# Kernel tuning notes

Measured on AMD Instinct MI355X. Metric: run time of the kernel, lower is better.

The kernel has to match this reference:

```python
import jax, jax.numpy as jnp
import numpy as np

N = 10000      # nodes (attention_adj_matrix_shape = (N, N))
E = 320000     # edges, avg degree 32
D_IN = 256     # input feature dim
D_H = 256      # hidden_units = [256]
ALPHA = 0.2    # leaky_relu slope for attention activation


def setup_inputs() -> dict:
    key = jax.random.key(0)
    k_x, k_src, k_dst, k_w1, k_b1, k_wa, k_ba = jax.random.split(key, 7)
    node_features = jax.random.normal(k_x, (N, D_IN), dtype=jnp.float32)
    # edges sorted by source column (tf.math.segment_sum requires sorted segment ids)
    src = jnp.sort(jax.random.randint(k_src, (E,), 0, N))
    dst = jax.random.randint(k_dst, (E,), 0, N)
    edges = jnp.stack([src, dst], axis=1).astype(jnp.int64)
    # hidden_layer: single Dense(256) (linear, keras Dense default activation=None)
    W1 = jax.random.normal(k_w1, (D_IN, D_H), dtype=jnp.float32) / np.sqrt(D_IN)
    b1 = jnp.zeros((D_H,), dtype=jnp.float32)
    # attention_layer: Dense(1) then activation
    Wa = jax.random.normal(k_wa, (2 * D_H, 1), dtype=jnp.float32) / np.sqrt(2 * D_H)
    ba = jnp.zeros((1,), dtype=jnp.float32)
    return {"node_features": node_features, "edges": edges,
            "W1": W1, "b1": b1, "Wa": Wa, "ba": ba}


def reference(node_features, edges, W1, b1, Wa, ba):
    n = node_features.shape[0]
    # hidden projection
    feats = node_features @ W1 + b1                       # [N, D_H]
    src, dst = edges[:, 0], edges[:, 1]
    # pairwise gather + concat: [E, 2*D_H]
    pair = jnp.concatenate([feats[src], feats[dst]], axis=1)
    scores = jax.nn.leaky_relu((pair @ Wa + ba)[:, 0], ALPHA)  # [E]
    # segment softmax over source node (matches exp / segment_sum / gather)
    ex = jnp.exp(scores)
    denom = jax.ops.segment_sum(ex, src, num_segments=n)       # [N]
    alpha = ex / denom[src]                                     # [E]
    # dense scatter of attention weights (scatter_nd sums duplicates)
    A = jnp.zeros((n, n), dtype=feats.dtype).at[src, dst].add(alpha)
    # add_self_features=False -> plain aggregate
    return A @ feats                                            # [N, D_H]
```

## Files before the change

### kernel.cpp

```cpp
#include <hip/hip_runtime.h>
#include <hip/hip_bf16.h>

#define N_NODES 10000
#define E_EDGES 320000
#define D 256
#define LRELU_ALPHA 0.2f


using short8  = __attribute__((ext_vector_type(8))) short;
using floatx4 = __attribute__((ext_vector_type(4))) float;
using bf16 = __hip_bfloat16;

__device__ __forceinline__ float bu2f(unsigned short u) {
    return __uint_as_float((unsigned)u << 16);
}

__global__ __launch_bounds__(256) void prep(const int* __restrict__ raw,
                                            int* __restrict__ dst,
                                            int* __restrict__ row_start) {
    bool is64 = true;
    #pragma unroll
    for (int t = 0; t < 16; ++t)
        if (raw[2 * t + 1] != 0) is64 = false;

    int e = blockIdx.x * 256 + threadIdx.x;
    if (e >= E_EDGES) return;
    int s, d, sprev;
    if (is64) { s = raw[4 * e]; d = raw[4 * e + 2]; sprev = e ? raw[4 * e - 4] : -1; }
    else      { s = raw[2 * e]; d = raw[2 * e + 1]; sprev = e ? raw[2 * e - 2] : -1; }
    dst[e] = d;
    for (int r = sprev + 1; r <= s; ++r) row_start[r] = e;
    if (e == E_EDGES - 1)
        for (int r = s + 1; r <= N_NODES; ++r) row_start[r] = E_EDGES;
}

__global__ __launch_bounds__(256) void xcast(const float* __restrict__ X,
                                             bf16* __restrict__ Xb) {
    const int i4 = blockIdx.x * 256 + threadIdx.x;
    const float4 v = ((const float4*)X)[i4];
    bf16* o = Xb + (size_t)i4 * 4;
    o[0] = __float2bfloat16(v.x);
    o[1] = __float2bfloat16(v.y);
    o[2] = __float2bfloat16(v.z);
    o[3] = __float2bfloat16(v.w);
}

__global__ __launch_bounds__(256) void wprep(const float* __restrict__ W1,
                                             bf16* __restrict__ W1f) {
    const int id = blockIdx.x * 256 + threadIdx.x;
    const int j = id & 7, l = (id >> 3) & 63, t = (id >> 9) & 15, s = id >> 13;
    const int k = s * 32 + (l >> 4) * 8 + j;
    const int n = t * 16 + (l & 15);
    W1f[id] = __float2bfloat16(W1[k * D + n]);
}

__global__ __launch_bounds__(256) void gemm_mfma(const bf16* __restrict__ Xb,
                                                 const bf16* __restrict__ W1f,
                                                 const float* __restrict__ b1,
                                                 const float* __restrict__ Wa,
                                                 bf16* __restrict__ featsb,
                                                 float* __restrict__ a_src,
                                                 float* __restrict__ a_dst) {
    const int w = threadIdx.x >> 6, l = threadIdx.x & 63;
    const int quad = l >> 4, lan = l & 15;
    const int row0 = blockIdx.x * 16;

    floatx4 acc[4] = {{0.f, 0.f, 0.f, 0.f}, {0.f, 0.f, 0.f, 0.f},
                      {0.f, 0.f, 0.f, 0.f}, {0.f, 0.f, 0.f, 0.f}};

    const short8* A8 = (const short8*)(Xb + (size_t)(row0 + lan) * D);
    const short8* B8 = (const short8*)W1f;

    #pragma unroll
    for (int s = 0; s < 8; ++s) {
        const short8 af = A8[s * 4 + quad];
        #pragma unroll
        for (int t = 0; t < 4; ++t) {
            const short8 bf = B8[(s * 16 + (4 * w + t)) * 64 + l];
            acc[t] = __builtin_amdgcn_mfma_f32_16x16x32_bf16(af, bf, acc[t], 0, 0, 0);
        }
    }

    float p1[4] = {0.f, 0.f, 0.f, 0.f}, p2[4] = {0.f, 0.f, 0.f, 0.f};
    #pragma unroll
    for (int t = 0; t < 4; ++t) {
        const int n = (4 * w + t) * 16 + lan;
        const float bias = b1[n], wa1 = Wa[n], wa2 = Wa[D + n];
        #pragma unroll
        for (int r = 0; r < 4; ++r) {
            const float v = acc[t][r] + bias;
            featsb[(size_t)(row0 + quad * 4 + r) * D + n] = __float2bfloat16(v);
            p1[r] += v * wa1;
            p2[r] += v * wa2;
        }
    }

    __shared__ float red1[4][16], red2[4][16];
    #pragma unroll
    for (int r = 0; r < 4; ++r) {
        #pragma unroll
        for (int off = 1; off < 16; off <<= 1) {
            p1[r] += __shfl_xor(p1[r], off);
            p2[r] += __shfl_xor(p2[r], off);
        }
        if (lan == 0) { red1[w][quad * 4 + r] = p1[r]; red2[w][quad * 4 + r] = p2[r]; }
    }
    __syncthreads();
    if (threadIdx.x < 16) {
        const int m = threadIdx.x;
        a_src[row0 + m] = red1[0][m] + red1[1][m] + red1[2][m] + red1[3][m];
        a_dst[row0 + m] = red2[0][m] + red2[1][m] + red2[2][m] + red2[3][m];
    }
}

__global__ __launch_bounds__(256) void aggregate(const int* __restrict__ dst,
                                                 const int* __restrict__ row_start,
                                                 const float* __restrict__ a_src,
                                                 const float* __restrict__ a_dst,
                                                 const float* __restrict__ ba,
                                                 const unsigned short* __restrict__ featsb,
                                                 float* __restrict__ out) {
    const int i = blockIdx.x * 4 + (threadIdx.x >> 6);
    const int l = threadIdx.x & 63;
    const int rs = row_start[i], re = row_start[i + 1];
    const float base = a_src[i] + ba[0];
    const ushort4* F = (const ushort4*)featsb;

    float4 acc = {0.f, 0.f, 0.f, 0.f};
    float dsum = 0.f;

    int e = rs;
    for (; e + 4 <= re; e += 4) {
        const int d0 = dst[e], d1 = dst[e + 1], d2 = dst[e + 2], d3 = dst[e + 3];
        const ushort4 f0 = F[(size_t)d0 * 64 + l];
        const ushort4 f1 = F[(size_t)d1 * 64 + l];
        const ushort4 f2 = F[(size_t)d2 * 64 + l];
        const ushort4 f3 = F[(size_t)d3 * 64 + l];
        float s0 = base + a_dst[d0]; s0 = (s0 > 0.f) ? s0 : LRELU_ALPHA * s0;
        float s1 = base + a_dst[d1]; s1 = (s1 > 0.f) ? s1 : LRELU_ALPHA * s1;
        float s2 = base + a_dst[d2]; s2 = (s2 > 0.f) ? s2 : LRELU_ALPHA * s2;
        float s3 = base + a_dst[d3]; s3 = (s3 > 0.f) ? s3 : LRELU_ALPHA * s3;
        const float x0 = expf(s0), x1 = expf(s1), x2 = expf(s2), x3 = expf(s3);
        acc.x += x0 * bu2f(f0.x) + x1 * bu2f(f1.x) + x2 * bu2f(f2.x) + x3 * bu2f(f3.x);
        acc.y += x0 * bu2f(f0.y) + x1 * bu2f(f1.y) + x2 * bu2f(f2.y) + x3 * bu2f(f3.y);
        acc.z += x0 * bu2f(f0.z) + x1 * bu2f(f1.z) + x2 * bu2f(f2.z) + x3 * bu2f(f3.z);
        acc.w += x0 * bu2f(f0.w) + x1 * bu2f(f1.w) + x2 * bu2f(f2.w) + x3 * bu2f(f3.w);
        dsum += x0 + x1 + x2 + x3;
    }
    for (; e < re; ++e) {
        const int d = dst[e];
        const ushort4 f = F[(size_t)d * 64 + l];
        float s = base + a_dst[d]; s = (s > 0.f) ? s : LRELU_ALPHA * s;
        const float x = expf(s);
        acc.x += x * bu2f(f.x); acc.y += x * bu2f(f.y);
        acc.z += x * bu2f(f.z); acc.w += x * bu2f(f.w);
        dsum += x;
    }

    const float inv = (re > rs) ? 1.f / dsum : 0.f;
    float4 o;
    o.x = acc.x * inv; o.y = acc.y * inv; o.z = acc.z * inv; o.w = acc.w * inv;
    ((float4*)out)[(size_t)i * 64 + l] = o;
}

extern "C" void kernel_launch(void* const* d_in, const int* in_sizes, int n_in,
                              void* d_out, int out_size, void* d_ws, size_t ws_size,
                              hipStream_t stream) {
    const float* X     = (const float*)d_in[0];
    const int*   edges = (const int*)d_in[1];
    const float* W1    = (const float*)d_in[2];
    const float* b1    = (const float*)d_in[3];
    const float* Wa    = (const float*)d_in[4];
    const float* ba    = (const float*)d_in[5];
    float* out = (float*)d_out;

    bf16* featsb = (bf16*)d_ws;
    bf16* Xb     = featsb + (size_t)N_NODES * D;
    bf16* W1f    = Xb + (size_t)N_NODES * D;
    float* a_src = (float*)(W1f + 65536);
    float* a_dst = a_src + N_NODES;
    int*   dstv  = (int*)(a_dst + N_NODES);
    int*   row_start = dstv + E_EDGES;

    prep<<<(E_EDGES + 255) / 256, 256, 0, stream>>>(edges, dstv, row_start);
    xcast<<<(N_NODES * D / 4) / 256, 256, 0, stream>>>(X, Xb);
    wprep<<<65536 / 256, 256, 0, stream>>>(W1, W1f);
    gemm_mfma<<<N_NODES / 16, 256, 0, stream>>>(Xb, W1f, b1, Wa, featsb, a_src, a_dst);
    aggregate<<<N_NODES / 4, 256, 0, stream>>>(dstv, row_start, a_src, a_dst, ba,
                                               (const unsigned short*)featsb, out);
}
```

Measured before the change: 112.1 us.

## Fuse X bf16 cast into GEMM and split aggregation into two feature halves

```diff
diff --git a/kernel.cpp b/kernel.cpp
--- a/kernel.cpp
+++ b/kernel.cpp
@@ -13,6 +13,11 @@
 
 __device__ __forceinline__ float bu2f(unsigned short u) {
     return __uint_as_float((unsigned)u << 16);
+}
+__device__ __forceinline__ unsigned short f2bu(float f) {
+    union { bf16 b; unsigned short u; } cv;
+    cv.b = __float2bfloat16(f);
+    return cv.u;
 }
 
 __global__ __launch_bounds__(256) void prep(const int* __restrict__ raw,
@@ -34,17 +39,6 @@
         for (int r = s + 1; r <= N_NODES; ++r) row_start[r] = E_EDGES;
 }
 
-__global__ __launch_bounds__(256) void xcast(const float* __restrict__ X,
-                                             bf16* __restrict__ Xb) {
-    const int i4 = blockIdx.x * 256 + threadIdx.x;
-    const float4 v = ((const float4*)X)[i4];
-    bf16* o = Xb + (size_t)i4 * 4;
-    o[0] = __float2bfloat16(v.x);
-    o[1] = __float2bfloat16(v.y);
-    o[2] = __float2bfloat16(v.z);
-    o[3] = __float2bfloat16(v.w);
-}
-
 __global__ __launch_bounds__(256) void wprep(const float* __restrict__ W1,
                                              bf16* __restrict__ W1f) {
     const int id = blockIdx.x * 256 + threadIdx.x;
@@ -54,7 +48,7 @@
     W1f[id] = __float2bfloat16(W1[k * D + n]);
 }
 
-__global__ __launch_bounds__(256) void gemm_mfma(const bf16* __restrict__ Xb,
+__global__ __launch_bounds__(256) void gemm_mfma(const float* __restrict__ X,
                                                  const bf16* __restrict__ W1f,
                                                  const float* __restrict__ b1,
                                                  const float* __restrict__ Wa,
@@ -68,12 +62,18 @@
     floatx4 acc[4] = {{0.f, 0.f, 0.f, 0.f}, {0.f, 0.f, 0.f, 0.f},
                       {0.f, 0.f, 0.f, 0.f}, {0.f, 0.f, 0.f, 0.f}};
 
-    const short8* A8 = (const short8*)(Xb + (size_t)(row0 + lan) * D);
+    const float4* Ax = (const float4*)(X + (size_t)(row0 + lan) * D);
     const short8* B8 = (const short8*)W1f;
 
     #pragma unroll
     for (int s = 0; s < 8; ++s) {
-        const short8 af = A8[s * 4 + quad];
+        const float4 u = Ax[s * 8 + quad * 2];
+        const float4 v = Ax[s * 8 + quad * 2 + 1];
+        short8 af;
+        af[0] = (short)f2bu(u.x); af[1] = (short)f2bu(u.y);
+        af[2] = (short)f2bu(u.z); af[3] = (short)f2bu(u.w);
+        af[4] = (short)f2bu(v.x); af[5] = (short)f2bu(v.y);
+        af[6] = (short)f2bu(v.z); af[7] = (short)f2bu(v.w);
         #pragma unroll
         for (int t = 0; t < 4; ++t) {
             const short8 bf = B8[(s * 16 + (4 * w + t)) * 64 + l];
@@ -113,54 +113,59 @@
     }
 }
 
-__global__ __launch_bounds__(256) void aggregate(const int* __restrict__ dst,
-                                                 const int* __restrict__ row_start,
-                                                 const float* __restrict__ a_src,
-                                                 const float* __restrict__ a_dst,
-                                                 const float* __restrict__ ba,
-                                                 const unsigned short* __restrict__ featsb,
-                                                 float* __restrict__ out) {
+__global__ __launch_bounds__(256) void aggregate_half(const int* __restrict__ dst,
+                                                      const int* __restrict__ row_start,
+                                                      const float* __restrict__ a_src,
+                                                      const float* __restrict__ a_dst,
+                                                      const float* __restrict__ ba,
+                                                      const unsigned short* __restrict__ featsb,
+                                                      float* __restrict__ out,
+                                                      const int half) {
     const int i = blockIdx.x * 4 + (threadIdx.x >> 6);
     const int l = threadIdx.x & 63;
     const int rs = row_start[i], re = row_start[i + 1];
     const float base = a_src[i] + ba[0];
-    const ushort4* F = (const ushort4*)featsb;
+    const unsigned int* F = (const unsigned int*)featsb;
+    const int off = half * 64 + l;
 
-    float4 acc = {0.f, 0.f, 0.f, 0.f};
+    float2 acc = {0.f, 0.f};
     float dsum = 0.f;
 
     int e = rs;
-    for (; e + 4 <= re; e += 4) {
-        const int d0 = dst[e], d1 = dst[e + 1], d2 = dst[e + 2], d3 = dst[e + 3];
-        const ushort4 f0 = F[(size_t)d0 * 64 + l];
-        const ushort4 f1 = F[(size_t)d1 * 64 + l];
-        const ushort4 f2 = F[(size_t)d2 * 64 + l];
-        const ushort4 f3 = F[(size_t)d3 * 64 + l];
-        float s0 = base + a_dst[d0]; s0 = (s0 > 0.f) ? s0 : LRELU_ALPHA * s0;
-        float s1 = base + a_dst[d1]; s1 = (s1 > 0.f) ? s1 : LRELU_ALPHA * s1;
-        float s2 = base + a_dst[d2]; s2 = (s2 > 0.f) ? s2 : LRELU_ALPHA * s2;
-        float s3 = base + a_dst[d3]; s3 = (s3 > 0.f) ? s3 : LRELU_ALPHA * s3;
-        const float x0 = expf(s0), x1 = expf(s1), x2 = expf(s2), x3 = expf(s3);
-        acc.x += x0 * bu2f(f0.x) + x1 * bu2f(f1.x) + x2 * bu2f(f2.x) + x3 * bu2f(f3.x);
-        acc.y += x0 * bu2f(f0.y) + x1 * bu2f(f1.y) + x2 * bu2f(f2.y) + x3 * bu2f(f3.y);
-        acc.z += x0 * bu2f(f0.z) + x1 * bu2f(f1.z) + x2 * bu2f(f2.z) + x3 * bu2f(f3.z);
-        acc.w += x0 * bu2f(f0.w) + x1 * bu2f(f1.w) + x2 * bu2f(f2.w) + x3 * bu2f(f3.w);
-        dsum += x0 + x1 + x2 + x3;
+    for (; e + 8 <= re; e += 8) {
+        unsigned int fw[8];
+        float xv[8];
+        #pragma unroll
+        for (int u = 0; u < 8; ++u) {
+            const int d = dst[e + u];
+            fw[u] = F[(size_t)d * 128 + off];
+            float s = base + a_dst[d];
+            s = (s > 0.f) ? s : LRELU_ALPHA * s;
+            xv[u] = expf(s);
+        }
+        #pragma unroll
+        for (int u = 0; u < 8; ++u) {
+            acc.x += xv[u] * bu2f((unsigned short)(fw[u] & 0xffff));
+            acc.y += xv[u] * bu2f((unsigned short)(fw[u] >> 16));
+            dsum += xv[u];
+        }
     }
     for (; e < re; ++e) {
         const int d = dst[e];
-        const ushort4 f = F[(size_t)d * 64 + l];
-        float s = base + a_dst[d]; s = (s > 0.f) ? s : LRELU_ALPHA * s;
+        const unsigned int f = F[(size_t)d * 128 + off];
+        float s = base + a_dst[d];
+        s = (s > 0.f) ? s : LRELU_ALPHA * s;
         const float x = expf(s);
-        acc.x += x * bu2f(f.x); acc.y += x * bu2f(f.y);
-        acc.z += x * bu2f(f.z); acc.w += x * bu2f(f.w);
+        acc.x += x * bu2f((unsigned short)(f & 0xffff));
+        acc.y += x * bu2f((unsigned short)(f >> 16));
         dsum += x;
     }
 
     const float inv = (re > rs) ? 1.f / dsum : 0.f;
-    float4 o;
-    o.x = acc.x * inv; o.y = acc.y * inv; o.z = acc.z * inv; o.w = acc.w * inv;
-    ((float4*)out)[(size_t)i * 64 + l] = o;
+    float2 o;
+    o.x = acc.x * inv;
+    o.y = acc.y * inv;
+    ((float2*)out)[(size_t)i * 128 + off] = o;
 }
 
 extern "C" void kernel_launch(void* const* d_in, const int* in_sizes, int n_in,
@@ -175,17 +180,17 @@
     float* out = (float*)d_out;
 
     bf16* featsb = (bf16*)d_ws;
-    bf16* Xb     = featsb + (size_t)N_NODES * D;
-    bf16* W1f    = Xb + (size_t)N_NODES * D;
+    bf16* W1f    = featsb + (size_t)N_NODES * D;
     float* a_src = (float*)(W1f + 65536);
     float* a_dst = a_src + N_NODES;
     int*   dstv  = (int*)(a_dst + N_NODES);
     int*   row_start = dstv + E_EDGES;
 
     prep<<<(E_EDGES + 255) / 256, 256, 0, stream>>>(edges, dstv, row_start);
-    xcast<<<(N_NODES * D / 4) / 256, 256, 0, stream>>>(X, Xb);
     wprep<<<65536 / 256, 256, 0, stream>>>(W1, W1f);
-    gemm_mfma<<<N_NODES / 16, 256, 0, stream>>>(Xb, W1f, b1, Wa, featsb, a_src, a_dst);
-    aggregate<<<N_NODES / 4, 256, 0, stream>>>(dstv, row_start, a_src, a_dst, ba,
-                                               (const unsigned short*)featsb, out);
+    gemm_mfma<<<N_NODES / 16, 256, 0, stream>>>(X, W1f, b1, Wa, featsb, a_src, a_dst);
+    aggregate_half<<<N_NODES / 4, 256, 0, stream>>>(dstv, row_start, a_src, a_dst, ba,
+                                                    (const unsigned short*)featsb, out, 0);
+    aggregate_half<<<N_NODES / 4, 256, 0, stream>>>(dstv, row_start, a_src, a_dst, ba,
+                                                    (const unsigned short*)featsb, out, 1);
 }
```

Result: slower. 123.0 us (+9.8%).
